# Optimization experiments

Measured on AMD Instinct MI355X. Metric: run time of the kernel, lower is better.

Reference implementation:

```python
import jax, jax.numpy as jnp
import numpy as np

EMBED_DIM = 1024
NUM_HEADS = 16
HEAD_DIM = EMBED_DIM // NUM_HEADS


def setup_inputs() -> dict:
    key = jax.random.key(0)
    kx, kq, kk, kv, ko = jax.random.split(key, 5)
    scale = 1.0 / np.sqrt(EMBED_DIM)
    return {
        "x": jax.random.normal(kx, (4, 2048, EMBED_DIM), dtype=jnp.float32),
        # nn.Linear weights are [out, in]; y = x @ W.T
        "w_q": jax.random.normal(kq, (EMBED_DIM, EMBED_DIM), dtype=jnp.float32) * scale,
        "w_k": jax.random.normal(kk, (EMBED_DIM, EMBED_DIM), dtype=jnp.float32) * scale,
        "w_v": jax.random.normal(kv, (EMBED_DIM, EMBED_DIM), dtype=jnp.float32) * scale,
        "w_o": jax.random.normal(ko, (EMBED_DIM, EMBED_DIM), dtype=jnp.float32) * scale,
    }


def reference(x, w_q, w_k, w_v, w_o):
    b, s, _ = x.shape
    # projections (Linear with no bias: x @ W.T)
    q = (x @ w_q.T).reshape(b, s, NUM_HEADS, HEAD_DIM).transpose(0, 2, 1, 3)
    k = (x @ w_k.T).reshape(b, s, NUM_HEADS, HEAD_DIM).transpose(0, 2, 1, 3)
    v = (x @ w_v.T).reshape(b, s, NUM_HEADS, HEAD_DIM).transpose(0, 2, 1, 3)
    # scores: [b, h, s, s]
    scores = jnp.einsum("bhqd,bhkd->bhqk", q, k) / jnp.sqrt(jnp.float32(HEAD_DIM)).astype(x.dtype)
    attn = jax.nn.softmax(scores, axis=-1)
    out = jnp.einsum("bhqk,bhkd->bhqd", attn, v)  # [b, h, s, d]
    out = out.transpose(0, 2, 1, 3).reshape(b, s, EMBED_DIM)
    return out @ w_o.T
```

## Files before the change

### kernel.cpp

```cpp
#include <hip/hip_runtime.h>
#include <math.h>

#define EMBED 1024
#define NHEAD 16
#define HDIM  64
#define BATCH 4
#define SEQ   2048
#define MROWS (BATCH * SEQ)

typedef __attribute__((ext_vector_type(4))) short short4v;
typedef __attribute__((ext_vector_type(8))) short short8;
typedef __attribute__((ext_vector_type(4))) float floatx4;
typedef __attribute__((ext_vector_type(16))) float floatx16;
typedef __attribute__((ext_vector_type(2))) unsigned uint2v;

#if __has_builtin(__builtin_amdgcn_exp2f)
#define EXP2(x) __builtin_amdgcn_exp2f(x)
#else
#define EXP2(x) exp2f(x)
#endif

__device__ __forceinline__ unsigned short f2bf(float f) {
  unsigned u = __float_as_uint(f);
  u += 0x7fffu + ((u >> 16) & 1u);
  return (unsigned short)(u >> 16);
}

#if __has_builtin(__builtin_amdgcn_cvt_pk_bf16_f32)
__device__ __forceinline__ unsigned pack2bf(float lo, float hi) {
  typedef __attribute__((ext_vector_type(2))) __bf16 bf2;
  union { bf2 b; unsigned u; } c;
  c.b = __builtin_amdgcn_cvt_pk_bf16_f32(lo, hi);
  return c.u;
}
#else
__device__ __forceinline__ unsigned pack2bf(float lo, float hi) {
  return ((__float_as_uint(lo) + 0x8000u) >> 16) |
         ((__float_as_uint(hi) + 0x8000u) & 0xffff0000u);
}
#endif

__device__ __forceinline__ uint2v pl32swap(unsigned a, unsigned b) {
#if __has_builtin(__builtin_amdgcn_permlane32_swap)
  return __builtin_amdgcn_permlane32_swap(a, b, false, false);
#else
  uint2v r;
  unsigned ax = (unsigned)__shfl_xor((int)a, 32);
  unsigned bx = (unsigned)__shfl_xor((int)b, 32);
  const int hi = (int)((threadIdx.x & 63) >> 5);
  r[0] = hi ? bx : a;
  r[1] = hi ? b : ax;
  return r;
#endif
}

__device__ __forceinline__ void gl_lds16(const void* g, void* l) {
  __builtin_amdgcn_global_load_lds(
      (const __attribute__((address_space(1))) unsigned int*)g,
      (__attribute__((address_space(3))) unsigned int*)l, 16, 0, 0);
}

__global__ __launch_bounds__(256) void cast_bf16_kernel(
    const float* __restrict__ x,  const float* __restrict__ wq,
    const float* __restrict__ wk, const float* __restrict__ wv,
    const float* __restrict__ wo,
    unsigned short* __restrict__ xb, unsigned short* __restrict__ wb) {
  const size_t NX = (size_t)MROWS * EMBED;
  size_t i4 = ((size_t)blockIdx.x * 256 + threadIdx.x) * 4;
  const float* src;
  unsigned short* dst;
  size_t off;
  if (i4 < NX) {
    src = x; dst = xb; off = i4;
  } else {
    size_t j = i4 - NX;
    int r = (int)(j >> 20);
    off = j & ((1u << 20) - 1);
    src = (r == 0) ? wq : (r == 1) ? wk : (r == 2) ? wv : wo;
    dst = wb + ((size_t)r << 20);
  }
  float4 v = *(const float4*)(src + off);
  ushort4 o;
  o.x = f2bf(v.x); o.y = f2bf(v.y); o.z = f2bf(v.z); o.w = f2bf(v.w);
  *(ushort4*)(dst + off) = o;
}

#define RD_A(bo, mi, ks) (*(const short8*)&LA[(bo) + wr * 8192 + \
    ((mi) * 16 + l15) * 64 + ((((ks) * 4 + quad) ^ (l15 & 7)) * 8)])
#define RD_B(boB, ni, ks) (*(const short8*)&LB[(boB) + \
    (rB0 + (ni) * 16 + l15) * 64 + ((((ks) * 4 + quad) ^ (l15 & 7)) * 8)])

__device__ __forceinline__ void gemm_core8(
    const unsigned short* __restrict__ Amat,
    const unsigned short* __restrict__ Bmat,
    int mBase, int nBase,
    unsigned short* LA, unsigned short* LB,
    floatx4 acc[8][2]) {
  const int t = threadIdx.x;
  const int lane = t & 63, wv = t >> 6;
  const int wr = wv >> 2, wc = wv & 3;
  const int quad = lane >> 4, l15 = lane & 15;
  const int rB0 = wc * 32;

  const unsigned short* sA[2][2];
  const unsigned short* sB[2];
  unsigned short* dA[2][2];
  unsigned short* dB[2];
#pragma unroll
  for (int i = 0; i < 2; ++i) {
    const int c = i * 512 + t;
    const int row = c >> 3, g = (c & 7) ^ (row & 7);
    sA[0][i] = Amat + (size_t)(mBase + row) * EMBED + g * 8;
    sA[1][i] = Amat + (size_t)(mBase + 128 + row) * EMBED + g * 8;
    sB[i]    = Bmat + (size_t)(nBase + row) * EMBED + g * 8;
    const int du = (i * 512 + wv * 64) * 8;
    dA[0][i] = LA + du;
    dA[1][i] = LA + 8192 + du;
    dB[i]    = LB + du;
  }

  gl_lds16(sA[0][0], dA[0][0]); gl_lds16(sA[0][1], dA[0][1]);
  gl_lds16(sA[1][0], dA[1][0]); gl_lds16(sA[1][1], dA[1][1]);
  gl_lds16(sB[0], dB[0]);       gl_lds16(sB[1], dB[1]);
  gl_lds16(sB[0] + 64, dB[0] + 8192);
  gl_lds16(sB[1] + 64, dB[1] + 8192);

  short8 b[2][2];
  for (int T = 0; T < 16; T += 2) {
#pragma unroll
    for (int hf = 0; hf < 2; ++hf) {
      const int bo = hf * 16384;
      const int boB = hf * 8192;
#pragma unroll
      for (int p = 0; p < 4; ++p) {
        short8 a[2][2];
        const int mi0 = 2 * p;
        if (p == 0) {
          {
            const int ts = (T + 1 + hf) & 15, tb = (ts & 1) * 16384;
            gl_lds16(sA[0][0] + (size_t)ts * 64, dA[0][0] + tb);
            gl_lds16(sA[0][1] + (size_t)ts * 64, dA[0][1] + tb);
          }
          asm volatile("s_waitcnt vmcnt(4)" ::: "memory");
          __builtin_amdgcn_sched_barrier(0);
          __builtin_amdgcn_s_barrier();
          b[0][0] = RD_B(boB, 0, 0); b[0][1] = RD_B(boB, 0, 1);
          b[1][0] = RD_B(boB, 1, 0); b[1][1] = RD_B(boB, 1, 1);
          a[0][0] = RD_A(bo, 0, 0); a[0][1] = RD_A(bo, 0, 1);
          a[1][0] = RD_A(bo, 1, 0); a[1][1] = RD_A(bo, 1, 1);
        } else {
          a[0][0] = RD_A(bo, mi0, 0);     a[0][1] = RD_A(bo, mi0, 1);
          a[1][0] = RD_A(bo, mi0 + 1, 0); a[1][1] = RD_A(bo, mi0 + 1, 1);
          if (p == 1) {
            const int ts = (T + 1 + hf) & 15, tb = (ts & 1) * 16384;
            gl_lds16(sA[1][0] + (size_t)ts * 64, dA[1][0] + tb);
            gl_lds16(sA[1][1] + (size_t)ts * 64, dA[1][1] + tb);
          } else if (p == 2) {
            const int ts = (T + 2 + hf) & 15, tbB = (ts & 1) * 8192;
            gl_lds16(sB[0] + (size_t)ts * 64, dB[0] + tbB);
            gl_lds16(sB[1] + (size_t)ts * 64, dB[1] + tbB);
          }
          __builtin_amdgcn_sched_barrier(0);
          __builtin_amdgcn_s_barrier();
        }
        asm volatile("s_waitcnt lgkmcnt(0)" ::: "memory");
        __builtin_amdgcn_sched_barrier(0);
        __builtin_amdgcn_s_setprio(1);
#pragma unroll
        for (int m2 = 0; m2 < 2; ++m2)
#pragma unroll
          for (int ni = 0; ni < 2; ++ni) {
            acc[mi0 + m2][ni] = __builtin_amdgcn_mfma_f32_16x16x32_bf16(
                a[m2][0], b[ni][0], acc[mi0 + m2][ni], 0, 0, 0);
            acc[mi0 + m2][ni] = __builtin_amdgcn_mfma_f32_16x16x32_bf16(
                a[m2][1], b[ni][1], acc[mi0 + m2][ni], 0, 0, 0);
          }
        __builtin_amdgcn_s_setprio(0);
        __builtin_amdgcn_sched_barrier(0);
        __builtin_amdgcn_s_barrier();
      }
    }
  }
  asm volatile("s_waitcnt vmcnt(0)" ::: "memory");
}

__global__ __launch_bounds__(512, 2) void proj_qkv_bf16(
    const unsigned short* __restrict__ xb,
    const unsigned short* __restrict__ wb,
    unsigned short* __restrict__ qkv) {
  const int id = blockIdx.x;
  const int xcd = id & 7;
  const int r = id >> 3;
  const int nIdx = r >> 2;
  const int mBase = (xcd * 4 + (r & 3)) * 256;
  const int nBase = nIdx * 128;

  __shared__ unsigned short LA[32768];
  __shared__ unsigned short LB[16384];

  floatx4 acc[8][2] = {};
  gemm_core8(xb, wb, mBase, nBase, LA, LB, acc);

  const int t = threadIdx.x;
  const int lane = t & 63, wv = t >> 6;
  const int wr = wv >> 2, wc = wv & 3;
  const int quad = lane >> 4, l15 = lane & 15;

  const int which = nBase >> 10;
  const int nloc0 = nBase & 1023;
  unsigned short* out = qkv + (size_t)which * MROWS * EMBED;

  if (which < 2) {
    const float scale = (which == 0) ? 0.18033688f : 1.0f;
#pragma unroll
    for (int mi = 0; mi < 8; ++mi)
#pragma unroll
      for (int ni = 0; ni < 2; ++ni) {
        const int nn = nloc0 + wc * 32 + ni * 16 + l15;
        const int h = nn >> 6, d = nn & 63;
#pragma unroll
        for (int r2 = 0; r2 < 4; ++r2) {
          const int m = mBase + wr * 128 + mi * 16 + quad * 4 + r2;
          const int b = m >> 11, s = m & (SEQ - 1);
          out[(((size_t)(b * NHEAD + h) * SEQ) + s) * HDIM + d] =
              f2bf(acc[mi][ni][r2] * scale);
        }
      }
  } else {
#pragma unroll
    for (int mi = 0; mi < 8; ++mi) {
      const int m0 = mBase + wr * 128 + mi * 16 + quad * 4;
      const int b = m0 >> 11, s0 = m0 & (SEQ - 1);
#pragma unroll
      for (int ni = 0; ni < 2; ++ni) {
        const int nn = nloc0 + wc * 32 + ni * 16 + l15;
        const int h = nn >> 6, d = nn & 63;
        ushort4 pk;
        pk.x = f2bf(acc[mi][ni][0]); pk.y = f2bf(acc[mi][ni][1]);
        pk.z = f2bf(acc[mi][ni][2]); pk.w = f2bf(acc[mi][ni][3]);
        *(ushort4*)&out[((size_t)(b * NHEAD + h) * HDIM + d) * SEQ + s0] = pk;
      }
    }
  }
}

__global__ __launch_bounds__(256, 2) void attn_mfma(
    const unsigned short* __restrict__ qkv,
    unsigned short* __restrict__ aout) {
  const unsigned short* Q = qkv;
  const unsigned short* K = qkv + (size_t)MROWS * EMBED;
  const unsigned short* V = qkv + 2 * (size_t)MROWS * EMBED;

  const int id = blockIdx.x;
  const int xcd = id & 7, slot = id >> 3;
  const int bh = xcd * 8 + (slot >> 3);
  const int qBase = (slot & 7) * 256;

  __shared__ unsigned short Ks[2 * 128 * 64];
  __shared__ unsigned short Vs[2 * 64 * 128];

  const int t = threadIdx.x;
  const int lane = t & 63, w = t >> 6;
  const int h2 = lane >> 5;
  const int q31 = lane & 31;

  const unsigned short* qrowA =
      Q + ((size_t)bh * SEQ + qBase + w * 64 + q31) * HDIM;
  const unsigned short* qrowB = qrowA + 32 * HDIM;
  short8 qaA[4], qaB[4];
#pragma unroll
  for (int ds = 0; ds < 4; ++ds) {
    qaA[ds] = *(const short8*)(qrowA + ds * 16 + h2 * 8);
    qaB[ds] = *(const short8*)(qrowB + ds * 16 + h2 * 8);
  }

  const unsigned short* kbase = K + (size_t)bh * SEQ * HDIM;
  const unsigned short* vbase = V + (size_t)bh * HDIM * SEQ;
  const unsigned short* gk[4];
  const unsigned short* gv[4];
  unsigned short* lk[4];
  unsigned short* lv[4];
#pragma unroll
  for (int i = 0; i < 4; ++i) {
    const int c = i * 256 + t;
    const int krow = c >> 3, kgrp = (c & 7) ^ (krow & 7);
    gk[i] = kbase + (size_t)krow * HDIM + kgrp * 8;
    const int vd = c >> 4, vj = (c & 15) ^ (vd & 15);
    gv[i] = vbase + (size_t)vd * SEQ + vj * 8;
    const int cu = i * 256 + w * 64;
    lk[i] = Ks + cu * 8;
    lv[i] = Vs + cu * 8;
  }

  floatx16 otA0 = {}, otA1 = {};
  floatx16 otB0 = {}, otB1 = {};
  float laccA = 0.0f, laccB = 0.0f;

#pragma unroll
  for (int i = 0; i < 4; ++i) {
    gl_lds16(gk[i], lk[i]);
    gl_lds16(gv[i], lv[i]);
  }

  for (int kt = 0; kt < SEQ; kt += 128) {
    const int cb = (kt >> 7) & 1;
    const int nb = cb ^ 1;
    const int nxt = (kt + 128) & (SEQ - 1);
    const int sOff = nb * 8192;
#pragma unroll
    for (int i = 0; i < 4; ++i) {
      gl_lds16(gk[i] + (size_t)nxt * HDIM, lk[i] + sOff);
      gl_lds16(gv[i] + nxt, lv[i] + sOff);
    }
    __builtin_amdgcn_sched_barrier(0);
    asm volatile("s_waitcnt vmcnt(8)" ::: "memory");
    __builtin_amdgcn_s_barrier();

    const int kOff = cb * 8192;
    const int vOff = cb * 8192;

#pragma unroll
    for (int sub = 0; sub < 2; ++sub) {
      const int koff = sub * 64;

      floatx16 stA0 = {}, stA1 = {}, stB0 = {}, stB1 = {};
      __builtin_amdgcn_s_setprio(1);
#pragma unroll
      for (int ds = 0; ds < 4; ++ds) {
        const int g = ds * 2 + h2;
        const int k0 = koff + q31;
        short8 ka0 = *(const short8*)&Ks[kOff + k0 * 64 + ((g ^ (q31 & 7)) * 8)];
        stA0 = __builtin_amdgcn_mfma_f32_32x32x16_bf16(ka0, qaA[ds], stA0, 0, 0, 0);
        stB0 = __builtin_amdgcn_mfma_f32_32x32x16_bf16(ka0, qaB[ds], stB0, 0, 0, 0);
        const int k1 = koff + 32 + q31;
        short8 ka1 = *(const short8*)&Ks[kOff + k1 * 64 + ((g ^ (q31 & 7)) * 8)];
        stA1 = __builtin_amdgcn_mfma_f32_32x32x16_bf16(ka1, qaA[ds], stA1, 0, 0, 0);
        stB1 = __builtin_amdgcn_mfma_f32_32x32x16_bf16(ka1, qaB[ds], stB1, 0, 0, 0);
      }
      __builtin_amdgcn_s_setprio(0);

      unsigned pkA0[8], pkA1[8], pkB0[8], pkB1[8];
#pragma unroll
      for (int i = 0; i < 8; ++i) {
        float a0 = EXP2(stA0[2 * i]), b0 = EXP2(stA0[2 * i + 1]);
        float a1 = EXP2(stA1[2 * i]), b1 = EXP2(stA1[2 * i + 1]);
        laccA += (a0 + b0) + (a1 + b1);
        pkA0[i] = pack2bf(a0, b0);
        pkA1[i] = pack2bf(a1, b1);
        float c0 = EXP2(stB0[2 * i]), d0 = EXP2(stB0[2 * i + 1]);
        float c1 = EXP2(stB1[2 * i]), d1 = EXP2(stB1[2 * i + 1]);
        laccB += (c0 + d0) + (c1 + d1);
        pkB0[i] = pack2bf(c0, d0);
        pkB1[i] = pack2bf(c1, d1);
      }

      __builtin_amdgcn_s_setprio(1);
#pragma unroll
      for (int sp = 0; sp < 4; ++sp) {
        const unsigned* pA = (sp < 2) ? pkA0 : pkA1;
        const unsigned* pB = (sp < 2) ? pkB0 : pkB1;
        const int off = (sp & 1) * 4;
        uint2v ra0 = pl32swap(pA[off + 0], pA[off + 2]);
        uint2v ra1 = pl32swap(pA[off + 1], pA[off + 3]);
        uint2v rb0 = pl32swap(pB[off + 0], pB[off + 2]);
        uint2v rb1 = pl32swap(pB[off + 1], pB[off + 3]);
        union { unsigned u[4]; short8 v; } pbA, pbB;
        pbA.u[0] = ra0[0]; pbA.u[1] = ra1[0]; pbA.u[2] = ra0[1]; pbA.u[3] = ra1[1];
        pbB.u[0] = rb0[0]; pbB.u[1] = rb1[0]; pbB.u[2] = rb0[1]; pbB.u[3] = rb1[1];

        const int g8 = sub * 8 + sp * 2 + h2;
        const int pos = (g8 ^ (q31 & 15)) * 8;
        short8 va0 = *(const short8*)&Vs[vOff + q31 * 128 + pos];
        otA0 = __builtin_amdgcn_mfma_f32_32x32x16_bf16(va0, pbA.v, otA0, 0, 0, 0);
        otB0 = __builtin_amdgcn_mfma_f32_32x32x16_bf16(va0, pbB.v, otB0, 0, 0, 0);
        short8 va1 = *(const short8*)&Vs[vOff + (32 + q31) * 128 + pos];
        otA1 = __builtin_amdgcn_mfma_f32_32x32x16_bf16(va1, pbA.v, otA1, 0, 0, 0);
        otB1 = __builtin_amdgcn_mfma_f32_32x32x16_bf16(va1, pbB.v, otB1, 0, 0, 0);
      }
      __builtin_amdgcn_s_setprio(0);
    }

    __builtin_amdgcn_sched_barrier(0);
    __builtin_amdgcn_s_barrier();
  }
  asm volatile("s_waitcnt vmcnt(0)" ::: "memory");

  const float totA = laccA + __shfl_xor(laccA, 32);
  const float totB = laccB + __shfl_xor(laccB, 32);
  const float invA = 1.0f / totA;
  const float invB = 1.0f / totB;

  const int b = bh >> 4, hh = bh & 15;
  unsigned short* orowA =
      aout + ((size_t)b * SEQ + qBase + w * 64 + q31) * EMBED + hh * HDIM;
  unsigned short* orowB = orowA + (size_t)32 * EMBED;
#pragma unroll
  for (int rg = 0; rg < 4; ++rg) {
    const int d0 = rg * 8 + h2 * 4;
    ushort4 p0, p1;
    p0.x = f2bf(otA0[4 * rg + 0] * invA); p0.y = f2bf(otA0[4 * rg + 1] * invA);
    p0.z = f2bf(otA0[4 * rg + 2] * invA); p0.w = f2bf(otA0[4 * rg + 3] * invA);
    *(ushort4*)(orowA + d0) = p0;
    p1.x = f2bf(otA1[4 * rg + 0] * invA); p1.y = f2bf(otA1[4 * rg + 1] * invA);
    p1.z = f2bf(otA1[4 * rg + 2] * invA); p1.w = f2bf(otA1[4 * rg + 3] * invA);
    *(ushort4*)(orowA + 32 + d0) = p1;
    ushort4 p2, p3;
    p2.x = f2bf(otB0[4 * rg + 0] * invB); p2.y = f2bf(otB0[4 * rg + 1] * invB);
    p2.z = f2bf(otB0[4 * rg + 2] * invB); p2.w = f2bf(otB0[4 * rg + 3] * invB);
    *(ushort4*)(orowB + d0) = p2;
    p3.x = f2bf(otB1[4 * rg + 0] * invB); p3.y = f2bf(otB1[4 * rg + 1] * invB);
    p3.z = f2bf(otB1[4 * rg + 2] * invB); p3.w = f2bf(otB1[4 * rg + 3] * invB);
    *(ushort4*)(orowB + 32 + d0) = p3;
  }
}

__global__ __launch_bounds__(512, 2) void out_proj_bf16(
    const unsigned short* __restrict__ aout,
    const unsigned short* __restrict__ wb,
    float* __restrict__ Cout) {
  const int id = blockIdx.x;
  const int xcd = id & 7;
  const int r = id >> 3;
  const int nBase = (r >> 2) * 128;
  const int mBase = (xcd * 4 + (r & 3)) * 256;

  __shared__ unsigned short LA[32768];
  __shared__ unsigned short LB[16384];

  floatx4 acc[8][2] = {};
  gemm_core8(aout, wb + ((size_t)3 << 20), mBase, nBase, LA, LB, acc);

  const int t = threadIdx.x;
  const int lane = t & 63, wv = t >> 6;
  const int wr = wv >> 2, wc = wv & 3;
  const int quad = lane >> 4, l15 = lane & 15;

#pragma unroll
  for (int mi = 0; mi < 8; ++mi)
#pragma unroll
    for (int ni = 0; ni < 2; ++ni) {
      const int n = nBase + wc * 32 + ni * 16 + l15;
#pragma unroll
      for (int r2 = 0; r2 < 4; ++r2) {
        const int m = mBase + wr * 128 + mi * 16 + quad * 4 + r2;
        Cout[(size_t)m * EMBED + n] = acc[mi][ni][r2];
      }
    }
}

extern "C" void kernel_launch(void* const* d_in, const int* in_sizes, int n_in,
                              void* d_out, int out_size, void* d_ws, size_t ws_size,
                              hipStream_t stream) {
  const float* x  = (const float*)d_in[0];
  const float* wq = (const float*)d_in[1];
  const float* wk = (const float*)d_in[2];
  const float* wv = (const float*)d_in[3];
  const float* wo = (const float*)d_in[4];
  float* out = (float*)d_out;

  char* ws = (char*)d_ws;
  unsigned short* xb   = (unsigned short*)(ws);
  unsigned short* wb   = (unsigned short*)(ws + (16u << 20));
  unsigned short* qkv  = (unsigned short*)(ws + (26u << 20));
  unsigned short* aout = (unsigned short*)(ws + (76u << 20));

  cast_bf16_kernel<<<12288, 256, 0, stream>>>(x, wq, wk, wv, wo, xb, wb);
  proj_qkv_bf16<<<768, 512, 0, stream>>>(xb, wb, qkv);
  attn_mfma<<<512, 256, 0, stream>>>(qkv, aout);
  out_proj_bf16<<<256, 512, 0, stream>>>(aout, wb, out);
}
```

Before: 265.7 us.

## Restructure QKV GEMM main loop into two larger MFMA phases per K-tile

The QKV projection GEMM main loop goes from four small sub-phases per half-tile, each with its own barrier, to two phases per K-tile that each load four A fragments and issue sixteen MFMAs. All A-tile prefetches are now issued at the top of the iteration, B prefetch follows the first phase, and the vmcnt wait becomes 6. The aim is fewer barriers and lgkmcnt waits per K-step and longer uninterrupted MFMA runs. The cost is more live fragment registers and less interleaving of LDS reads with math, which could hurt occupancy or hiding of LDS latency.

```diff
diff --git a/kernel.cpp b/kernel.cpp
--- a/kernel.cpp
+++ b/kernel.cpp
@@ -125,61 +125,70 @@
   gl_lds16(sB[0] + 64, dB[0] + 8192);
   gl_lds16(sB[1] + 64, dB[1] + 8192);
 
-  short8 b[2][2];
-  for (int T = 0; T < 16; T += 2) {
-#pragma unroll
-    for (int hf = 0; hf < 2; ++hf) {
-      const int bo = hf * 16384;
-      const int boB = hf * 8192;
-#pragma unroll
-      for (int p = 0; p < 4; ++p) {
-        short8 a[2][2];
-        const int mi0 = 2 * p;
-        if (p == 0) {
-          {
-            const int ts = (T + 1 + hf) & 15, tb = (ts & 1) * 16384;
-            gl_lds16(sA[0][0] + (size_t)ts * 64, dA[0][0] + tb);
-            gl_lds16(sA[0][1] + (size_t)ts * 64, dA[0][1] + tb);
-          }
-          asm volatile("s_waitcnt vmcnt(4)" ::: "memory");
-          __builtin_amdgcn_sched_barrier(0);
-          __builtin_amdgcn_s_barrier();
-          b[0][0] = RD_B(boB, 0, 0); b[0][1] = RD_B(boB, 0, 1);
-          b[1][0] = RD_B(boB, 1, 0); b[1][1] = RD_B(boB, 1, 1);
-          a[0][0] = RD_A(bo, 0, 0); a[0][1] = RD_A(bo, 0, 1);
-          a[1][0] = RD_A(bo, 1, 0); a[1][1] = RD_A(bo, 1, 1);
-        } else {
-          a[0][0] = RD_A(bo, mi0, 0);     a[0][1] = RD_A(bo, mi0, 1);
-          a[1][0] = RD_A(bo, mi0 + 1, 0); a[1][1] = RD_A(bo, mi0 + 1, 1);
-          if (p == 1) {
-            const int ts = (T + 1 + hf) & 15, tb = (ts & 1) * 16384;
-            gl_lds16(sA[1][0] + (size_t)ts * 64, dA[1][0] + tb);
-            gl_lds16(sA[1][1] + (size_t)ts * 64, dA[1][1] + tb);
-          } else if (p == 2) {
-            const int ts = (T + 2 + hf) & 15, tbB = (ts & 1) * 8192;
-            gl_lds16(sB[0] + (size_t)ts * 64, dB[0] + tbB);
-            gl_lds16(sB[1] + (size_t)ts * 64, dB[1] + tbB);
-          }
-          __builtin_amdgcn_sched_barrier(0);
-          __builtin_amdgcn_s_barrier();
-        }
-        asm volatile("s_waitcnt lgkmcnt(0)" ::: "memory");
-        __builtin_amdgcn_sched_barrier(0);
-        __builtin_amdgcn_s_setprio(1);
-#pragma unroll
-        for (int m2 = 0; m2 < 2; ++m2)
-#pragma unroll
-          for (int ni = 0; ni < 2; ++ni) {
-            acc[mi0 + m2][ni] = __builtin_amdgcn_mfma_f32_16x16x32_bf16(
-                a[m2][0], b[ni][0], acc[mi0 + m2][ni], 0, 0, 0);
-            acc[mi0 + m2][ni] = __builtin_amdgcn_mfma_f32_16x16x32_bf16(
-                a[m2][1], b[ni][1], acc[mi0 + m2][ni], 0, 0, 0);
-          }
-        __builtin_amdgcn_s_setprio(0);
-        __builtin_amdgcn_sched_barrier(0);
-        __builtin_amdgcn_s_barrier();
-      }
-    }
+  for (int T = 0; T < 16; ++T) {
+    const int bo  = (T & 1) * 16384;
+    const int boB = (T & 1) * 8192;
+
+    {
+      const int ts = (T + 1) & 15, tb = (ts & 1) * 16384;
+      gl_lds16(sA[0][0] + (size_t)ts * 64, dA[0][0] + tb);
+      gl_lds16(sA[0][1] + (size_t)ts * 64, dA[0][1] + tb);
+      gl_lds16(sA[1][0] + (size_t)ts * 64, dA[1][0] + tb);
+      gl_lds16(sA[1][1] + (size_t)ts * 64, dA[1][1] + tb);
+    }
+    asm volatile("s_waitcnt vmcnt(6)" ::: "memory");
+    __builtin_amdgcn_sched_barrier(0);
+    __builtin_amdgcn_s_barrier();
+
+    short8 b0[2][2], a[4][2];
+    b0[0][0] = RD_B(boB, 0, 0); b0[0][1] = RD_B(boB, 0, 1);
+    b0[1][0] = RD_B(boB, 1, 0); b0[1][1] = RD_B(boB, 1, 1);
+#pragma unroll
+    for (int mi = 0; mi < 4; ++mi) {
+      a[mi][0] = RD_A(bo, mi, 0);
+      a[mi][1] = RD_A(bo, mi, 1);
+    }
+    asm volatile("s_waitcnt lgkmcnt(0)" ::: "memory");
+    __builtin_amdgcn_sched_barrier(0);
+    __builtin_amdgcn_s_setprio(1);
+#pragma unroll
+    for (int mi = 0; mi < 4; ++mi)
+#pragma unroll
+      for (int ni = 0; ni < 2; ++ni) {
+        acc[mi][ni] = __builtin_amdgcn_mfma_f32_16x16x32_bf16(
+            a[mi][0], b0[ni][0], acc[mi][ni], 0, 0, 0);
+        acc[mi][ni] = __builtin_amdgcn_mfma_f32_16x16x32_bf16(
+            a[mi][1], b0[ni][1], acc[mi][ni], 0, 0, 0);
+      }
+    __builtin_amdgcn_s_setprio(0);
+    __builtin_amdgcn_sched_barrier(0);
+    __builtin_amdgcn_s_barrier();
+
+    {
+      const int ts = (T + 2) & 15, tbB = (ts & 1) * 8192;
+      gl_lds16(sB[0] + (size_t)ts * 64, dB[0] + tbB);
+      gl_lds16(sB[1] + (size_t)ts * 64, dB[1] + tbB);
+    }
+#pragma unroll
+    for (int mi = 0; mi < 4; ++mi) {
+      a[mi][0] = RD_A(bo, 4 + mi, 0);
+      a[mi][1] = RD_A(bo, 4 + mi, 1);
+    }
+    asm volatile("s_waitcnt lgkmcnt(0)" ::: "memory");
+    __builtin_amdgcn_sched_barrier(0);
+    __builtin_amdgcn_s_setprio(1);
+#pragma unroll
+    for (int mi = 0; mi < 4; ++mi)
+#pragma unroll
+      for (int ni = 0; ni < 2; ++ni) {
+        acc[4 + mi][ni] = __builtin_amdgcn_mfma_f32_16x16x32_bf16(
+            a[mi][0], b0[ni][0], acc[4 + mi][ni], 0, 0, 0);
+        acc[4 + mi][ni] = __builtin_amdgcn_mfma_f32_16x16x32_bf16(
+            a[mi][1], b0[ni][1], acc[4 + mi][ni], 0, 0, 0);
+      }
+    __builtin_amdgcn_s_setprio(0);
+    __builtin_amdgcn_sched_barrier(0);
+    __builtin_amdgcn_s_barrier();
   }
   asm volatile("s_waitcnt vmcnt(0)" ::: "memory");
 }
```

After: 269.8 us. No clear change (+1.5%).
